# Kernel tuning notes

Hardware: AMD Instinct MI355X
Metric: run time of the kernel (lower is better)

The kernel has to match this reference:

```python
import jax, jax.numpy as jnp
import numpy as np

TEMPERATURE = 1.0

def setup_inputs() -> dict:
    key = jax.random.key(0)
    k1, k2 = jax.random.split(key)
    N, D = 8192, 128
    embeddings = jax.random.normal(k1, (N, D), dtype=jnp.float32)
    labels = jax.random.randint(k2, (N,), 0, 2, dtype=jnp.int64)
    return {"embeddings": embeddings, "labels": labels}

def reference(embeddings, labels):
    # L2-normalize rows (F.normalize p=2, dim=1)
    e = embeddings / jnp.linalg.norm(embeddings, axis=1, keepdims=True)
    N = e.shape[0]
    # scaled similarities; log of the exp'd matrix in the original is just `sim`
    sim = (e @ e.T) / TEMPERATURE            # [N, N]
    expS = jnp.exp(sim)
    eye = jnp.eye(N, dtype=bool)
    # denominator for row i: sum over all j != i of exp(sim_ij)
    # (off-diag same-class terms + all cross-class terms == all off-diag terms)
    denom = jnp.sum(jnp.where(eye, 0.0, expS), axis=1)   # [N]
    same = labels[:, None] == labels[None, :]
    pos_mask = same & ~eye                                # off-diagonal same-class pairs
    cnt = jnp.sum(pos_mask, axis=1).astype(sim.dtype)     # (#same-class - 1) per row
    # loss_i = -sum_{j in pos} (sim_ij - log denom_i)
    loss_i = -(jnp.sum(jnp.where(pos_mask, sim, 0.0), axis=1) - cnt * jnp.log(denom))
    is_pos = (labels == 0)
    num_pos = jnp.sum(is_pos).astype(sim.dtype)
    # Faithful to source: class-0 part averaged by num_pos, class-1 part added
    # un-averaged into the same accumulator; loss_neg stays 0.
    loss = jnp.sum(jnp.where(is_pos, loss_i, 0.0)) / num_pos \
         + jnp.sum(jnp.where(is_pos, 0.0, loss_i))
    return loss
```

## Files before the change

### kernel.cpp

```cpp
#include <hip/hip_runtime.h>
#include <hip/hip_bf16.h>

typedef float f32x4 __attribute__((ext_vector_type(4)));
typedef __bf16 bf16x8 __attribute__((ext_vector_type(8)));

#define D_DIM 128
#define NSPLIT 32
#define SCALE  1.2011224087864498f
#define LN2    0.6931471805599453f
#define E1     2.7182818284590452f

static __device__ __forceinline__ unsigned short f2bf(float f) {
    unsigned u = __float_as_uint(f);
    u += 0x7fffu + ((u >> 16) & 1u);
    return (unsigned short)(u >> 16);
}

static __device__ __forceinline__ void gload_lds16(const unsigned short* gsrc, unsigned short* lds_dst) {
    auto gp = (const __attribute__((address_space(1))) unsigned int*)gsrc;
    auto lp = (__attribute__((address_space(3))) unsigned int*)(unsigned int)(unsigned long long)lds_dst;
    __builtin_amdgcn_global_load_lds(gp, lp, 16, 0, 0);
}

__global__ __launch_bounds__(256) void prep_kernel(const float* __restrict__ X,
                                                   const int* __restrict__ labels,
                                                   unsigned short* __restrict__ A,
                                                   float* __restrict__ C,
                                                   int* __restrict__ n0) {
    __shared__ float CL[256];
    int tid = threadIdx.x, wave = tid >> 6, lane = tid & 63;
    CL[tid] = 0.0f;
    __syncthreads();

    int row0 = blockIdx.x * 64 + wave * 16;
    float c0x = 0.f, c0y = 0.f, c1x = 0.f, c1y = 0.f;
    int cnt0 = 0;
    for (int t = 0; t < 16; ++t) {
        int row = row0 + t;
        float2 v = *reinterpret_cast<const float2*>(X + (size_t)row * D_DIM + lane * 2);
        float ss = v.x * v.x + v.y * v.y;
        #pragma unroll
        for (int m = 32; m; m >>= 1) ss += __shfl_xor(ss, m);
        float rn = rsqrtf(ss) * SCALE;
        float a0 = v.x * rn, a1 = v.y * rn;
        ushort2 o; o.x = f2bf(a0); o.y = f2bf(a1);
        *reinterpret_cast<ushort2*>(A + (size_t)row * D_DIM + lane * 2) = o;
        bool is0 = (labels[row] == 0);
        c0x += is0 ? a0 : 0.f;  c0y += is0 ? a1 : 0.f;
        c1x += is0 ? 0.f : a0;  c1y += is0 ? 0.f : a1;
        if (lane == 0) cnt0 += is0 ? 1 : 0;
    }
    atomicAdd(&CL[lane * 2],           c0x);
    atomicAdd(&CL[lane * 2 + 1],       c0y);
    atomicAdd(&CL[128 + lane * 2],     c1x);
    atomicAdd(&CL[128 + lane * 2 + 1], c1y);
    if (lane == 0) atomicAdd(n0, cnt0);
    __syncthreads();
    atomicAdd(&C[tid], CL[tid]);
}

__global__ __launch_bounds__(256, 3) void main_kernel(const unsigned short* __restrict__ A,
                                                      float* __restrict__ S1part,
                                                      int N) {
    __shared__ unsigned short Bs[8192];
    int tid = threadIdx.x, wave = tid >> 6, lane = tid & 63;
    int l15 = lane & 15, lhi = lane >> 4;
    int m0 = blockIdx.x * 256 + wave * 64;
    int split = blockIdx.y;
    int j0 = split * (N / NSPLIT);
    const int TILES = (N / NSPLIT) / 64;

    bf16x8 af[4][4];
    const unsigned short* abase = A + (size_t)(m0 + l15) * D_DIM + lhi * 8;
    #pragma unroll
    for (int ms = 0; ms < 4; ++ms)
        #pragma unroll
        for (int kb = 0; kb < 4; ++kb)
            af[ms][kb] = *reinterpret_cast<const bf16x8*>(abase + (size_t)ms * 16 * D_DIM + kb * 32);

    float s1[4][4];
    #pragma unroll
    for (int ms = 0; ms < 4; ++ms)
        #pragma unroll
        for (int r = 0; r < 4; ++r) s1[ms][r] = 0.0f;

    int sw = (l15 & 7) << 4;
    const char* BsB = (const char*)Bs;

    for (int t = 0; t < TILES; ++t) {
        int jt = j0 + t * 64;
        #pragma unroll
        for (int it = 0; it < 4; ++it) {
            int Lb  = it * 4096 + tid * 16;
            int col = Lb >> 8;
            int off = (Lb & 255) ^ ((col & 7) << 4);
            const unsigned short* g = A + (size_t)(jt + col) * D_DIM + (off >> 1);
            gload_lds16(g, (unsigned short*)((char*)Bs + it * 4096 + wave * 1024));
        }
        __syncthreads();

        #pragma unroll
        for (int cs = 0; cs < 4; ++cs) {
            int colb = (cs * 16 + l15) * 256;
            bf16x8 bf[4];
            #pragma unroll
            for (int kb = 0; kb < 4; ++kb)
                bf[kb] = *reinterpret_cast<const bf16x8*>(BsB + colb + ((kb * 64 + lhi * 16) ^ sw));
            f32x4 acc[4] = {{0,0,0,0},{0,0,0,0},{0,0,0,0},{0,0,0,0}};
            #pragma unroll
            for (int kb = 0; kb < 4; ++kb)
                #pragma unroll
                for (int ms = 0; ms < 4; ++ms)
                    acc[ms] = __builtin_amdgcn_mfma_f32_16x16x32_bf16(af[ms][kb], bf[kb], acc[ms], 0, 0, 0);
            #pragma unroll
            for (int ms = 0; ms < 4; ++ms)
                #pragma unroll
                for (int r = 0; r < 4; ++r)
                    s1[ms][r] += __builtin_amdgcn_exp2f(acc[ms][r]);
        }
        __syncthreads();
    }

    #pragma unroll
    for (int m = 1; m < 16; m <<= 1)
        #pragma unroll
        for (int ms = 0; ms < 4; ++ms)
            #pragma unroll
            for (int r = 0; r < 4; ++r)
                s1[ms][r] += __shfl_xor(s1[ms][r], m);
    if (l15 == 0) {
        #pragma unroll
        for (int ms = 0; ms < 4; ++ms)
            #pragma unroll
            for (int r = 0; r < 4; ++r)
                S1part[(size_t)split * N + m0 + ms * 16 + lhi * 4 + r] = s1[ms][r];
    }
}

__global__ __launch_bounds__(256) void finish_kernel(const unsigned short* __restrict__ A,
                                                     const float* __restrict__ S1part,
                                                     const float* __restrict__ C,
                                                     const int* __restrict__ labels,
                                                     int* __restrict__ n0p,
                                                     float* __restrict__ scal,
                                                     int* __restrict__ counter,
                                                     float* __restrict__ out,
                                                     int N) {
    int tid = threadIdx.x;
    int row = blockIdx.x * 256 + tid;

    float S1 = 0.0f;
    for (int s = 0; s < NSPLIT; ++s) S1 += S1part[(size_t)s * N + row];
    int lab = labels[row];
    const float* Cl = C + (lab ? 128 : 0);
    float dot = 0.0f;
    #pragma unroll
    for (int kb = 0; kb < 16; ++kb) {
        bf16x8 a = *reinterpret_cast<const bf16x8*>(A + (size_t)row * D_DIM + kb * 8);
        #pragma unroll
        for (int e = 0; e < 8; ++e) dot += (float)a[e] * Cl[kb * 8 + e];
    }
    float s2 = dot * LN2;
    float lg = __builtin_amdgcn_logf(S1 - E1) * LN2;
    float p  = s2 - 1.0f;
    bool is0 = (lab == 0);
    float v[4] = { is0 ? lg : 0.0f, is0 ? 0.0f : lg, is0 ? p : 0.0f, is0 ? 0.0f : p };
    #pragma unroll
    for (int m = 32; m; m >>= 1)
        #pragma unroll
        for (int q = 0; q < 4; ++q) v[q] += __shfl_xor(v[q], m);

    __shared__ float red[4][4];
    int wave = tid >> 6, lane = tid & 63;
    if (lane == 0)
        #pragma unroll
        for (int q = 0; q < 4; ++q) red[wave][q] = v[q];
    __syncthreads();
    if (tid == 0) {
        float tt[4];
        #pragma unroll
        for (int q = 0; q < 4; ++q) tt[q] = red[0][q] + red[1][q] + red[2][q] + red[3][q];
        atomicAdd(&scal[0], tt[0]);
        atomicAdd(&scal[1], tt[1]);
        atomicAdd(&scal[2], tt[2]);
        atomicAdd(&scal[3], tt[3]);
        __threadfence();
        int old = atomicAdd(counter, 1);
        if (old == (int)gridDim.x - 1) {
            float L0 = atomicAdd(&scal[0], 0.0f);
            float L1 = atomicAdd(&scal[1], 0.0f);
            float P0 = atomicAdd(&scal[2], 0.0f);
            float P1 = atomicAdd(&scal[3], 0.0f);
            int n0 = atomicAdd(n0p, 0);
            float fn0 = (float)n0, fn1 = (float)(N - n0);
            float loss = ((fn0 - 1.0f) * L0 - P0) / fn0 + (fn1 - 1.0f) * L1 - P1;
            out[0] = loss;
        }
    }
}

extern "C" void kernel_launch(void* const* d_in, const int* in_sizes, int n_in,
                              void* d_out, int out_size, void* d_ws, size_t ws_size,
                              hipStream_t stream) {
    (void)n_in; (void)out_size; (void)ws_size;
    const float* X      = (const float*)d_in[0];
    const int*   labels = (const int*)d_in[1];
    int N = in_sizes[1];

    char* ws = (char*)d_ws;
    size_t A_bytes  = (size_t)N * D_DIM * 2;
    size_t S1_bytes = (size_t)NSPLIT * N * 4;
    unsigned short* A      = (unsigned short*)ws;
    float*          S1part = (float*)(ws + A_bytes);
    float*          C      = (float*)(ws + A_bytes + S1_bytes);
    float*          scal   = (float*)((char*)C + 1024);
    int*            n0     = (int*)((char*)scal + 16);
    int*            counter= (int*)((char*)n0 + 4);
    float*          out    = (float*)d_out;

    hipMemsetAsync(C, 0, 1024 + 16 + 4 + 4, stream);

    prep_kernel<<<N / 64, 256, 0, stream>>>(X, labels, A, C, n0);

    dim3 grid(N / 256, NSPLIT);
    main_kernel<<<grid, 256, 0, stream>>>(A, S1part, N);

    finish_kernel<<<N / 256, 256, 0, stream>>>(A, S1part, C, labels, n0, scal, counter, out, N);
}
```

Baseline: 121.3 us.

## Fuse finish into main kernel, double-buffer B tiles, drop memset

Removes the separate finish kernel and the memset. The main kernel now atomically accumulates row sums into S1, and the last block computes the final loss. The positive-pair sum is taken as the squared norm of the class centroid sums instead of a per-row dot product. Main-loop B tiles are double-buffered so the next tile's global-to-LDS load overlaps the MFMA work. The prep kernel uses wider vector loads and writes per-block partials instead of global atomics. This saves two launches and removes the S1part traffic, but adds global float atomics and a serial tail on one block.

```diff
diff --git a/kernel.cpp b/kernel.cpp
--- a/kernel.cpp
+++ b/kernel.cpp
@@ -1,14 +1,15 @@
 #include <hip/hip_runtime.h>
-#include <hip/hip_bf16.h>
 
 typedef float f32x4 __attribute__((ext_vector_type(4)));
 typedef __bf16 bf16x8 __attribute__((ext_vector_type(8)));
+typedef unsigned short u16x8 __attribute__((ext_vector_type(8)));
 
 #define D_DIM 128
 #define NSPLIT 32
+#define BJ 64
 #define SCALE  1.2011224087864498f
 #define LN2    0.6931471805599453f
-#define E1     2.7182818284590452f
+#define E1F    2.7182818284590452f
 
 static __device__ __forceinline__ unsigned short f2bf(float f) {
     unsigned u = __float_as_uint(f);
@@ -16,7 +17,7 @@
     return (unsigned short)(u >> 16);
 }
 
-static __device__ __forceinline__ void gload_lds16(const unsigned short* gsrc, unsigned short* lds_dst) {
+static __device__ __forceinline__ void gload_lds16(const unsigned short* gsrc, void* lds_dst) {
     auto gp = (const __attribute__((address_space(1))) unsigned int*)gsrc;
     auto lp = (__attribute__((address_space(3))) unsigned int*)(unsigned int)(unsigned long long)lds_dst;
     __builtin_amdgcn_global_load_lds(gp, lp, 16, 0, 0);
@@ -25,50 +26,78 @@
 __global__ __launch_bounds__(256) void prep_kernel(const float* __restrict__ X,
                                                    const int* __restrict__ labels,
                                                    unsigned short* __restrict__ A,
-                                                   float* __restrict__ C,
-                                                   int* __restrict__ n0) {
+                                                   float* __restrict__ Cpart,
+                                                   int* __restrict__ n0part,
+                                                   float* __restrict__ S1,
+                                                   int* __restrict__ counter) {
+    int tid = threadIdx.x, wave = tid >> 6, lane = tid & 63;
+    int g = lane >> 4, s = lane & 15;
+    int row0 = blockIdx.x * 64;
+
+    float c0[8], c1[8];
+    #pragma unroll
+    for (int e = 0; e < 8; ++e) { c0[e] = 0.f; c1[e] = 0.f; }
+
+    #pragma unroll
+    for (int it = 0; it < 4; ++it) {
+        int row = row0 + wave * 16 + it * 4 + g;
+        const float4* xp = reinterpret_cast<const float4*>(X + (size_t)row * D_DIM + s * 8);
+        float4 xa = xp[0], xb = xp[1];
+        float ss = xa.x*xa.x + xa.y*xa.y + xa.z*xa.z + xa.w*xa.w
+                 + xb.x*xb.x + xb.y*xb.y + xb.z*xb.z + xb.w*xb.w;
+        ss += __shfl_xor(ss, 1); ss += __shfl_xor(ss, 2);
+        ss += __shfl_xor(ss, 4); ss += __shfl_xor(ss, 8);
+        float rn = rsqrtf(ss) * SCALE;
+        float v[8] = { xa.x*rn, xa.y*rn, xa.z*rn, xa.w*rn,
+                       xb.x*rn, xb.y*rn, xb.z*rn, xb.w*rn };
+        u16x8 o;
+        #pragma unroll
+        for (int e = 0; e < 8; ++e) o[e] = f2bf(v[e]);
+        *reinterpret_cast<u16x8*>(A + (size_t)row * D_DIM + s * 8) = o;
+        bool is0 = (labels[row] == 0);
+        #pragma unroll
+        for (int e = 0; e < 8; ++e) {
+            c0[e] += is0 ? v[e] : 0.f;
+            c1[e] += is0 ? 0.f : v[e];
+        }
+    }
+
     __shared__ float CL[256];
-    int tid = threadIdx.x, wave = tid >> 6, lane = tid & 63;
-    CL[tid] = 0.0f;
-    __syncthreads();
-
-    int row0 = blockIdx.x * 64 + wave * 16;
-    float c0x = 0.f, c0y = 0.f, c1x = 0.f, c1y = 0.f;
-    int cnt0 = 0;
-    for (int t = 0; t < 16; ++t) {
-        int row = row0 + t;
-        float2 v = *reinterpret_cast<const float2*>(X + (size_t)row * D_DIM + lane * 2);
-        float ss = v.x * v.x + v.y * v.y;
-        #pragma unroll
-        for (int m = 32; m; m >>= 1) ss += __shfl_xor(ss, m);
-        float rn = rsqrtf(ss) * SCALE;
-        float a0 = v.x * rn, a1 = v.y * rn;
-        ushort2 o; o.x = f2bf(a0); o.y = f2bf(a1);
-        *reinterpret_cast<ushort2*>(A + (size_t)row * D_DIM + lane * 2) = o;
-        bool is0 = (labels[row] == 0);
-        c0x += is0 ? a0 : 0.f;  c0y += is0 ? a1 : 0.f;
-        c1x += is0 ? 0.f : a0;  c1y += is0 ? 0.f : a1;
-        if (lane == 0) cnt0 += is0 ? 1 : 0;
-    }
-    atomicAdd(&CL[lane * 2],           c0x);
-    atomicAdd(&CL[lane * 2 + 1],       c0y);
-    atomicAdd(&CL[128 + lane * 2],     c1x);
-    atomicAdd(&CL[128 + lane * 2 + 1], c1y);
-    if (lane == 0) atomicAdd(n0, cnt0);
-    __syncthreads();
-    atomicAdd(&C[tid], CL[tid]);
+    CL[tid] = 0.f;
+    __syncthreads();
+    #pragma unroll
+    for (int e = 0; e < 8; ++e) {
+        atomicAdd(&CL[s * 8 + e],       c0[e]);
+        atomicAdd(&CL[128 + s * 8 + e], c1[e]);
+    }
+    __syncthreads();
+    Cpart[(size_t)blockIdx.x * 256 + tid] = CL[tid];
+
+    if (wave == 0) {
+        int is0 = (labels[row0 + lane] == 0) ? 1 : 0;
+        unsigned long long b = __ballot(is0);
+        if (lane == 0) n0part[blockIdx.x] = (int)__popcll(b);
+    }
+    if (tid < 64) S1[row0 + tid] = 0.f;
+    if (blockIdx.x == 0 && tid == 0) *counter = 0;
 }
 
 __global__ __launch_bounds__(256, 3) void main_kernel(const unsigned short* __restrict__ A,
-                                                      float* __restrict__ S1part,
-                                                      int N) {
-    __shared__ unsigned short Bs[8192];
+                                                      const int* __restrict__ labels,
+                                                      const float* __restrict__ Cpart,
+                                                      const int* __restrict__ n0part,
+                                                      float* __restrict__ S1,
+                                                      int* __restrict__ counter,
+                                                      float* __restrict__ out,
+                                                      int N, int nprep) {
+    __shared__ unsigned short Bs[2][8192];
     int tid = threadIdx.x, wave = tid >> 6, lane = tid & 63;
     int l15 = lane & 15, lhi = lane >> 4;
     int m0 = blockIdx.x * 256 + wave * 64;
     int split = blockIdx.y;
-    int j0 = split * (N / NSPLIT);
-    const int TILES = (N / NSPLIT) / 64;
+    int jlen = N / NSPLIT;
+    int j0 = split * jlen;
+    const int TILES = jlen / BJ;
 
     bf16x8 af[4][4];
     const unsigned short* abase = A + (size_t)(m0 + l15) * D_DIM + lhi * 8;
@@ -82,36 +111,40 @@
     #pragma unroll
     for (int ms = 0; ms < 4; ++ms)
         #pragma unroll
-        for (int r = 0; r < 4; ++r) s1[ms][r] = 0.0f;
+        for (int r = 0; r < 4; ++r) s1[ms][r] = 0.f;
 
     int sw = (l15 & 7) << 4;
-    const char* BsB = (const char*)Bs;
-
-    for (int t = 0; t < TILES; ++t) {
-        int jt = j0 + t * 64;
+
+    auto stage = [&](int buf, int jt) {
         #pragma unroll
         for (int it = 0; it < 4; ++it) {
             int Lb  = it * 4096 + tid * 16;
             int col = Lb >> 8;
             int off = (Lb & 255) ^ ((col & 7) << 4);
-            const unsigned short* g = A + (size_t)(jt + col) * D_DIM + (off >> 1);
-            gload_lds16(g, (unsigned short*)((char*)Bs + it * 4096 + wave * 1024));
-        }
-        __syncthreads();
-
+            gload_lds16(A + (size_t)(jt + col) * D_DIM + (off >> 1),
+                        (char*)(&Bs[0][0]) + buf * 16384 + it * 4096 + wave * 1024);
+        }
+    };
+
+    stage(0, j0);
+    __syncthreads();
+    int buf = 0;
+    for (int t = 0; t < TILES; ++t) {
+        if (t + 1 < TILES) stage(buf ^ 1, j0 + (t + 1) * BJ);
+        const char* BsB = (const char*)(&Bs[0][0]) + buf * 16384;
         #pragma unroll
         for (int cs = 0; cs < 4; ++cs) {
             int colb = (cs * 16 + l15) * 256;
-            bf16x8 bf[4];
+            bf16x8 bfr[4];
             #pragma unroll
             for (int kb = 0; kb < 4; ++kb)
-                bf[kb] = *reinterpret_cast<const bf16x8*>(BsB + colb + ((kb * 64 + lhi * 16) ^ sw));
+                bfr[kb] = *reinterpret_cast<const bf16x8*>(BsB + colb + ((kb * 64 + lhi * 16) ^ sw));
             f32x4 acc[4] = {{0,0,0,0},{0,0,0,0},{0,0,0,0},{0,0,0,0}};
             #pragma unroll
             for (int kb = 0; kb < 4; ++kb)
                 #pragma unroll
                 for (int ms = 0; ms < 4; ++ms)
-                    acc[ms] = __builtin_amdgcn_mfma_f32_16x16x32_bf16(af[ms][kb], bf[kb], acc[ms], 0, 0, 0);
+                    acc[ms] = __builtin_amdgcn_mfma_f32_16x16x32_bf16(af[ms][kb], bfr[kb], acc[ms], 0, 0, 0);
             #pragma unroll
             for (int ms = 0; ms < 4; ++ms)
                 #pragma unroll
@@ -119,6 +152,7 @@
                     s1[ms][r] += __builtin_amdgcn_exp2f(acc[ms][r]);
         }
         __syncthreads();
+        buf ^= 1;
     }
 
     #pragma unroll
@@ -133,68 +167,51 @@
         for (int ms = 0; ms < 4; ++ms)
             #pragma unroll
             for (int r = 0; r < 4; ++r)
-                S1part[(size_t)split * N + m0 + ms * 16 + lhi * 4 + r] = s1[ms][r];
-    }
-}
-
-__global__ __launch_bounds__(256) void finish_kernel(const unsigned short* __restrict__ A,
-                                                     const float* __restrict__ S1part,
-                                                     const float* __restrict__ C,
-                                                     const int* __restrict__ labels,
-                                                     int* __restrict__ n0p,
-                                                     float* __restrict__ scal,
-                                                     int* __restrict__ counter,
-                                                     float* __restrict__ out,
-                                                     int N) {
-    int tid = threadIdx.x;
-    int row = blockIdx.x * 256 + tid;
-
-    float S1 = 0.0f;
-    for (int s = 0; s < NSPLIT; ++s) S1 += S1part[(size_t)s * N + row];
-    int lab = labels[row];
-    const float* Cl = C + (lab ? 128 : 0);
-    float dot = 0.0f;
-    #pragma unroll
-    for (int kb = 0; kb < 16; ++kb) {
-        bf16x8 a = *reinterpret_cast<const bf16x8*>(A + (size_t)row * D_DIM + kb * 8);
-        #pragma unroll
-        for (int e = 0; e < 8; ++e) dot += (float)a[e] * Cl[kb * 8 + e];
-    }
-    float s2 = dot * LN2;
-    float lg = __builtin_amdgcn_logf(S1 - E1) * LN2;
-    float p  = s2 - 1.0f;
-    bool is0 = (lab == 0);
-    float v[4] = { is0 ? lg : 0.0f, is0 ? 0.0f : lg, is0 ? p : 0.0f, is0 ? 0.0f : p };
-    #pragma unroll
-    for (int m = 32; m; m >>= 1)
-        #pragma unroll
-        for (int q = 0; q < 4; ++q) v[q] += __shfl_xor(v[q], m);
-
-    __shared__ float red[4][4];
-    int wave = tid >> 6, lane = tid & 63;
-    if (lane == 0)
-        #pragma unroll
-        for (int q = 0; q < 4; ++q) red[wave][q] = v[q];
+                atomicAdd(&S1[m0 + ms * 16 + lhi * 4 + r], s1[ms][r]);
+    }
+
+    __shared__ int isLast;
     __syncthreads();
     if (tid == 0) {
-        float tt[4];
-        #pragma unroll
-        for (int q = 0; q < 4; ++q) tt[q] = red[0][q] + red[1][q] + red[2][q] + red[3][q];
-        atomicAdd(&scal[0], tt[0]);
-        atomicAdd(&scal[1], tt[1]);
-        atomicAdd(&scal[2], tt[2]);
-        atomicAdd(&scal[3], tt[3]);
         __threadfence();
         int old = atomicAdd(counter, 1);
-        if (old == (int)gridDim.x - 1) {
-            float L0 = atomicAdd(&scal[0], 0.0f);
-            float L1 = atomicAdd(&scal[1], 0.0f);
-            float P0 = atomicAdd(&scal[2], 0.0f);
-            float P1 = atomicAdd(&scal[3], 0.0f);
-            int n0 = atomicAdd(n0p, 0);
+        isLast = (old == (int)(gridDim.x * gridDim.y) - 1) ? 1 : 0;
+    }
+    __syncthreads();
+    if (isLast) {
+        float csum = 0.f;
+        for (int b = 0; b < nprep; ++b) csum += Cpart[(size_t)b * 256 + tid];
+        float sq = csum * csum;
+        #pragma unroll
+        for (int m = 1; m < 64; m <<= 1) sq += __shfl_xor(sq, m);
+        int nv = (tid < nprep) ? n0part[tid] : 0;
+        #pragma unroll
+        for (int m = 1; m < 64; m <<= 1) nv += __shfl_xor(nv, m);
+        float l0 = 0.f, l1 = 0.f;
+        for (int i = tid; i < N; i += 256) {
+            float d  = S1[i] - E1F;
+            float lg = __builtin_amdgcn_logf(d) * LN2;
+            if (labels[i] == 0) l0 += lg; else l1 += lg;
+        }
+        #pragma unroll
+        for (int m = 1; m < 64; m <<= 1) { l0 += __shfl_xor(l0, m); l1 += __shfl_xor(l1, m); }
+
+        __shared__ float red[4][3];
+        __shared__ int   nred[4];
+        if (lane == 0) {
+            red[wave][0] = sq; red[wave][1] = l0; red[wave][2] = l1;
+            nred[wave] = nv;
+        }
+        __syncthreads();
+        if (tid == 0) {
+            float C0sq = (red[0][0] + red[1][0]) * LN2;
+            float C1sq = (red[2][0] + red[3][0]) * LN2;
+            float L0 = red[0][1] + red[1][1] + red[2][1] + red[3][1];
+            float L1 = red[0][2] + red[1][2] + red[2][2] + red[3][2];
+            int   n0 = nred[0] + nred[1] + nred[2] + nred[3];
             float fn0 = (float)n0, fn1 = (float)(N - n0);
-            float loss = ((fn0 - 1.0f) * L0 - P0) / fn0 + (fn1 - 1.0f) * L1 - P1;
-            out[0] = loss;
+            float P0 = C0sq - fn0, P1 = C1sq - fn1;
+            out[0] = ((fn0 - 1.f) * L0 - P0) / fn0 + (fn1 - 1.f) * L1 - P1;
         }
     }
 }
@@ -206,24 +223,18 @@
     const float* X      = (const float*)d_in[0];
     const int*   labels = (const int*)d_in[1];
     int N = in_sizes[1];
+    int nprep = N / 64;
 
     char* ws = (char*)d_ws;
-    size_t A_bytes  = (size_t)N * D_DIM * 2;
-    size_t S1_bytes = (size_t)NSPLIT * N * 4;
-    unsigned short* A      = (unsigned short*)ws;
-    float*          S1part = (float*)(ws + A_bytes);
-    float*          C      = (float*)(ws + A_bytes + S1_bytes);
-    float*          scal   = (float*)((char*)C + 1024);
-    int*            n0     = (int*)((char*)scal + 16);
-    int*            counter= (int*)((char*)n0 + 4);
-    float*          out    = (float*)d_out;
-
-    hipMemsetAsync(C, 0, 1024 + 16 + 4 + 4, stream);
-
-    prep_kernel<<<N / 64, 256, 0, stream>>>(X, labels, A, C, n0);
+    unsigned short* A       = (unsigned short*)ws;
+    float*          S1      = (float*)(ws + (size_t)N * D_DIM * 2);
+    float*          Cpart   = (float*)((char*)S1 + (size_t)N * 4);
+    int*            n0part  = (int*)((char*)Cpart + (size_t)nprep * 256 * 4);
+    int*            counter = n0part + nprep;
+    float*          out     = (float*)d_out;
+
+    prep_kernel<<<nprep, 256, 0, stream>>>(X, labels, A, Cpart, n0part, S1, counter);
 
     dim3 grid(N / 256, NSPLIT);
-    main_kernel<<<grid, 256, 0, stream>>>(A, S1part, N);
-
-    finish_kernel<<<N / 256, 256, 0, stream>>>(A, S1part, C, labels, n0, scal, counter, out, N);
-}
+    main_kernel<<<grid, 256, 0, stream>>>(A, labels, Cpart, n0part, S1, counter, out, N, nprep);
+}
```

Result: slower. 176.1 us (+45.2%).
